# Kernel optimization log

Measured on AMD Instinct MI355X. Metric: run time of the kernel, lower is better.

Reference implementation:

```python
import jax, jax.numpy as jnp
import numpy as np

N = 50000      # nodes
E = 800000     # edges (avg degree 16)
D = 128        # d_model
C = 2          # num_classes
F_IN = 8       # GCNConv(8, d_model)


def setup_inputs() -> dict:
    key = jax.random.key(0)
    ks = jax.random.split(key, 12)
    s = 0.05  # weight init scale
    return {
        "feature_vec": jax.random.normal(ks[0], (N, F_IN), dtype=jnp.float32),
        "bboxes": jax.random.uniform(ks[1], (N, 4), dtype=jnp.float32),
        "bbox_indices": jnp.arange(N, dtype=jnp.int64) if jax.config.jax_enable_x64 else jnp.arange(N, dtype=jnp.int32),
        "edge_index": jax.random.randint(ks[2], (2, E), 0, N, dtype=jnp.int32),
        "W1": jax.random.normal(ks[3], (F_IN, D), dtype=jnp.float32) * s,
        "b1": jnp.zeros((D,), dtype=jnp.float32),
        "W2": jax.random.normal(ks[4], (D, D), dtype=jnp.float32) * s,
        "b2": jnp.zeros((D,), dtype=jnp.float32),
        "lin1_W": jax.random.normal(ks[5], (2 * D, D), dtype=jnp.float32) * s,
        "lin1_b": jnp.zeros((D,), dtype=jnp.float32),
        "linf_W": jax.random.normal(ks[6], (D, C), dtype=jnp.float32) * s,
        "linf_b": jnp.zeros((C,), dtype=jnp.float32),
    }


def gcn_conv(x, W, b, edge_index, n):
    """PyG GCNConv: add self-loops, symmetric D^-1/2 A D^-1/2 normalization."""
    x = x @ W                                   # [n, out]
    sl = jnp.arange(n, dtype=edge_index.dtype)
    row = jnp.concatenate([edge_index[0], sl])  # source
    col = jnp.concatenate([edge_index[1], sl])  # target
    ones = jnp.ones(row.shape[0], dtype=x.dtype)
    deg = jax.ops.segment_sum(ones, col, num_segments=n)  # >= 1 due to self-loops
    dinv = jax.lax.rsqrt(deg)
    norm = dinv[row] * dinv[col]                # [E + n]
    msg = x[row] * norm[:, None]                # gather + scale
    out = jax.ops.segment_sum(msg, col, num_segments=n)   # scatter-aggregate
    return out + b


def reference(feature_vec, bboxes, bbox_indices, edge_index,
              W1, b1, W2, b2, lin1_W, lin1_b, linf_W, linf_b):
    n = feature_vec.shape[0]
    x = jax.nn.relu(gcn_conv(feature_vec, W1, b1, edge_index, n))
    x = jax.nn.relu(gcn_conv(x, W2, b2, edge_index, n))
    x1 = x[edge_index[0]]                        # [E, D]
    x2 = x[edge_index[1]]                        # [E, D]
    xpair = jnp.concatenate([x1, x2], axis=-1)   # [E, 2D]
    xpair = jax.nn.relu(xpair @ lin1_W + lin1_b)
    xfin = xpair @ linf_W + linf_b               # [E, C]
    probs = jax.nn.log_softmax(xfin, axis=-1)
    bbox_pairs = jnp.concatenate([bboxes[edge_index[0]], bboxes[edge_index[1]]], axis=-1)  # [E, 8]
    bbox_index_pairs = jnp.stack([bbox_indices[edge_index[0]], bbox_indices[edge_index[1]]], axis=1)  # [E, 2]
    return (probs, bbox_pairs, bbox_index_pairs)
```

## Files before the change

### kernel.cpp

```cpp
#include <hip/hip_runtime.h>
#include <hip/hip_bf16.h>
#include <math.h>


typedef __attribute__((ext_vector_type(8))) short short8;
typedef __attribute__((ext_vector_type(4))) float f32x4;
typedef __attribute__((ext_vector_type(2))) float fv2;

__device__ inline ushort f2bf(float f) {
    union { __hip_bfloat16 h; ushort u; } cv;
    cv.h = __float2bfloat16(f);
    return cv.u;
}
__device__ inline float bf2f(ushort u) {
    union { float f; uint u; } c;
    c.u = ((uint)u) << 16;
    return c.f;
}
__device__ inline uchar f2fp8(float f) {
    uint p = __builtin_amdgcn_cvt_pk_fp8_f32(f, f, 0u, false);
    return (uchar)(p & 0xffu);
}

__global__ void k_hist(const int* __restrict__ col, int* __restrict__ cnt, int E) {
    int e = blockIdx.x * blockDim.x + threadIdx.x;
    if (e < E) atomicAdd(&cnt[col[e]], 1);
}

__global__ __launch_bounds__(1024) void k_bsum(const int* __restrict__ cnt,
                                               int* __restrict__ bsum, int N) {
    __shared__ int ts[1024];
    const int b = blockIdx.x, t = threadIdx.x;
    const int i0 = b * 2048 + 2 * t;
    int a0 = (i0 < N) ? cnt[i0] : 0;
    int a1 = (i0 + 1 < N) ? cnt[i0 + 1] : 0;
    ts[t] = a0 + a1;
    __syncthreads();
#pragma unroll
    for (int off = 512; off > 0; off >>= 1) {
        if (t < off) ts[t] += ts[t + off];
        __syncthreads();
    }
    if (t == 0) bsum[b] = ts[0];
}

__global__ __launch_bounds__(1024) void k_scanw(const int* __restrict__ cnt,
                                                const int* __restrict__ bsum,
                                                int* __restrict__ ptr, int N, int E) {
    __shared__ int ts[1024];
    const int b = blockIdx.x, t = threadIdx.x;
    int boff = 0;
    for (int i = 0; i < b; ++i) boff += bsum[i];
    const int i0 = b * 2048 + 2 * t;
    const int a0 = (i0 < N) ? cnt[i0] : 0;
    const int a1 = (i0 + 1 < N) ? cnt[i0 + 1] : 0;
    const int s = a0 + a1;
    ts[t] = s;
    __syncthreads();
    for (int off = 1; off < 1024; off <<= 1) {
        int v = (t >= off) ? ts[t - off] : 0;
        __syncthreads();
        ts[t] += v;
        __syncthreads();
    }
    const int excl = boff + ts[t] - s;
    if (i0 < N) ptr[i0] = excl;
    if (i0 + 1 < N) ptr[i0 + 1] = excl + a0;
    if (b == 0 && t == 0) ptr[N] = E;
}

__global__ void k_fill(const int* __restrict__ row, const int* __restrict__ col,
                       const int* __restrict__ cnt, const int* __restrict__ ptr,
                       int* __restrict__ cursor, int2* __restrict__ eadj, int E) {
    int e = blockIdx.x * blockDim.x + threadIdx.x;
    if (e >= E) return;
    int r = row[e], c = col[e];
    float dr = rsqrtf(1.0f + (float)cnt[r]);
    float dc = rsqrtf(1.0f + (float)cnt[c]);
    int p = ptr[c] + atomicAdd(&cursor[c], 1);
    eadj[p] = make_int2(r, __float_as_int(dr * dc));
}

__global__ void k_prepWuv(const float* __restrict__ W, ushort* __restrict__ Wuv) {
    int tid = blockIdx.x * blockDim.x + threadIdx.x;
    if (tid >= 256 * 128) return;
    int c = tid >> 7, k = tid & 127;
    int krow = k + ((c >> 7) << 7);
    Wuv[tid] = f2bf(W[krow * 128 + (c & 127)]);
}
__global__ void k_prepW2(const float* __restrict__ W, ushort* __restrict__ Wt) {
    int tid = blockIdx.x * blockDim.x + threadIdx.x;
    if (tid >= 128 * 128) return;
    int n = tid >> 7, k = tid & 127;
    Wt[tid] = f2bf(W[k * 128 + n]);
}

__global__ __launch_bounds__(256) void k_agg8(const float* __restrict__ feat,
                                              const int* __restrict__ cnt,
                                              const int* __restrict__ ptr,
                                              const int2* __restrict__ eadj,
                                              float* __restrict__ aggF, int N) {
    int lane8 = threadIdx.x & 7;
    int node = blockIdx.x * 32 + (threadIdx.x >> 3);
    if (node >= N) return;
    float dd = 1.0f / (1.0f + (float)cnt[node]);
    float acc = feat[(size_t)node * 8 + lane8] * dd;
    int i = ptr[node], end = ptr[node + 1];
    for (; i < end; ++i) {
        const int2 a = eadj[i];
        acc += feat[(size_t)a.x * 8 + lane8] * __int_as_float(a.y);
    }
    aggF[(size_t)node * 8 + lane8] = acc;
}

__global__ __launch_bounds__(256) void k_gemm1(const float* __restrict__ aggF,
                                               const float* __restrict__ W1,
                                               const float* __restrict__ b1,
                                               ushort* __restrict__ x1, int total) {
    int tid = blockIdx.x * blockDim.x + threadIdx.x;
    if (tid >= total) return;
    int n = tid >> 7, j = tid & 127;
    float acc = b1[j];
#pragma unroll
    for (int k = 0; k < 8; ++k) acc += aggF[(size_t)n * 8 + k] * W1[k * 128 + j];
    x1[tid] = f2bf(fmaxf(acc, 0.f));
}

__global__ __launch_bounds__(256) void k_gemm2(const ushort* __restrict__ x1,
                                               const ushort* __restrict__ W2t,
                                               ushort* __restrict__ h2, int N) {
    __shared__ ushort ldsW[128 * 128];
    const int tid = threadIdx.x;
    const int wave = tid >> 6, lane = tid & 63;
    const int m = lane & 15, kb = lane >> 4;
    const int n0 = blockIdx.x * 64;

    const int node_a = min(n0 + wave * 16 + m, N - 1);
    short8 a[4];
#pragma unroll
    for (int kk = 0; kk < 4; ++kk) {
        a[kk] = *reinterpret_cast<const short8*>(&x1[(size_t)node_a * 128 + kk * 32 + kb * 8]);
    }

    {
        char* lb = reinterpret_cast<char*>(ldsW);
        const short8* wg = reinterpret_cast<const short8*>(W2t);
#pragma unroll
        for (int i = 0; i < 8; ++i) {
            const int g = i * 256 + tid;
            const int bo = g * 16;
            const int swz = bo ^ (((bo >> 8) & 7) << 4);
            *reinterpret_cast<short8*>(lb + swz) = wg[g];
        }
    }
    __syncthreads();

    f32x4 acc[8];
#pragma unroll
    for (int t = 0; t < 8; ++t) acc[t] = (f32x4){0.f, 0.f, 0.f, 0.f};

    const char* lbr = reinterpret_cast<const char*>(ldsW);
    const int mswz = (m & 7) << 4;
#pragma unroll
    for (int kk = 0; kk < 4; ++kk) {
#pragma unroll
        for (int t = 0; t < 8; ++t) {
            const int bo = (t * 16 + m) * 256 + kk * 64 + kb * 16;
            const short8 b = *reinterpret_cast<const short8*>(lbr + (bo ^ mswz));
            acc[t] = __builtin_amdgcn_mfma_f32_16x16x32_bf16(a[kk], b, acc[t], 0, 0, 0);
        }
    }

#pragma unroll
    for (int r = 0; r < 4; ++r) {
        const int node = n0 + wave * 16 + kb * 4 + r;
        if (node < N) {
#pragma unroll
            for (int t = 0; t < 8; ++t) {
                h2[(size_t)node * 128 + t * 16 + m] = f2bf(acc[t][r]);
            }
        }
    }
}

__global__ __launch_bounds__(256) void k_gather2(const ushort* __restrict__ h2,
                                                 const int* __restrict__ cnt,
                                                 const int* __restrict__ ptr,
                                                 const int2* __restrict__ eadj,
                                                 const float* __restrict__ b2,
                                                 ushort* __restrict__ xbf, int N) {
    int lane16 = threadIdx.x & 15;
    int node = blockIdx.x * 16 + (threadIdx.x >> 4);
    if (node >= N) return;
    float dd = 1.0f / (1.0f + (float)cnt[node]);
    float acc[8];
    {
        const short8 v = *reinterpret_cast<const short8*>(&h2[(size_t)node * 128 + lane16 * 8]);
#pragma unroll
        for (int i = 0; i < 8; ++i) acc[i] = bf2f((ushort)v[i]) * dd;
    }
    int i = ptr[node], end = ptr[node + 1];
    for (; i < end; ++i) {
        const int2 aa = eadj[i];
        const int s = aa.x;
        const float nm = __int_as_float(aa.y);
        const short8 v = *reinterpret_cast<const short8*>(&h2[(size_t)s * 128 + lane16 * 8]);
#pragma unroll
        for (int q = 0; q < 8; ++q) acc[q] += bf2f((ushort)v[q]) * nm;
    }
    short8 r;
#pragma unroll
    for (int q = 0; q < 8; ++q) {
        r[q] = (short)f2bf(fmaxf(acc[q] + b2[lane16 * 8 + q], 0.f));
    }
    *reinterpret_cast<short8*>(&xbf[(size_t)node * 128 + lane16 * 8]) = r;
}

__global__ __launch_bounds__(512) void k_gemm_uv(const ushort* __restrict__ xbf,
                                                 const ushort* __restrict__ Wuv,
                                                 const float* __restrict__ lin1b,
                                                 uchar* __restrict__ uv, int N) {
    __shared__ ushort ldsW[256 * 128];
    const int tid = threadIdx.x;
    const int wave = tid >> 6, lane = tid & 63;
    const int m = lane & 15, kb = lane >> 4;
    const int ng = wave >> 1;
    const int ch = wave & 1;
    const int n0 = blockIdx.x * 64 + ng * 16;

    const int node_a = min(n0 + m, N - 1);
    short8 a[4];
#pragma unroll
    for (int kk = 0; kk < 4; ++kk) {
        a[kk] = *reinterpret_cast<const short8*>(&xbf[(size_t)node_a * 128 + kk * 32 + kb * 8]);
    }

    {
        char* lb = reinterpret_cast<char*>(ldsW);
        const short8* wg = reinterpret_cast<const short8*>(Wuv);
#pragma unroll
        for (int i = 0; i < 8; ++i) {
            const int g = i * 512 + tid;
            const int bo = g * 16;
            const int swz = bo ^ (((bo >> 8) & 7) << 4);
            *reinterpret_cast<short8*>(lb + swz) = wg[g];
        }
    }
    __syncthreads();

    f32x4 acc[8];
#pragma unroll
    for (int t = 0; t < 8; ++t) acc[t] = (f32x4){0.f, 0.f, 0.f, 0.f};

    const char* lbr = reinterpret_cast<const char*>(ldsW);
    const int mswz = (m & 7) << 4;
#pragma unroll
    for (int kk = 0; kk < 4; ++kk) {
#pragma unroll
        for (int t = 0; t < 8; ++t) {
            const int bo = (ch * 128 + t * 16 + m) * 256 + kk * 64 + kb * 16;
            const short8 b = *reinterpret_cast<const short8*>(lbr + (bo ^ mswz));
            acc[t] = __builtin_amdgcn_mfma_f32_16x16x32_bf16(a[kk], b, acc[t], 0, 0, 0);
        }
    }

#pragma unroll
    for (int r = 0; r < 4; ++r) {
        const int node = n0 + kb * 4 + r;
        if (node < N) {
#pragma unroll
            for (int t = 0; t < 8; ++t) {
                const int c = t * 16 + m;
                float av = acc[t][r];
                if (ch == 0) av += lin1b[c];
                uv[(size_t)node * 256 + ch * 128 + c] = f2fp8(av);
            }
        }
    }
}

__global__ __launch_bounds__(256) void k_edge_lite(const uchar* __restrict__ uv,
                                                   const float* __restrict__ linfW,
                                                   const float* __restrict__ linfb,
                                                   const float* __restrict__ bboxes,
                                                   const int* __restrict__ bidx,
                                                   const int* __restrict__ row,
                                                   const int* __restrict__ col,
                                                   float* __restrict__ out_probs,
                                                   float* __restrict__ out_bbox,
                                                   float* __restrict__ out_bidx,
                                                   int E) {
    const int lane8 = threadIdx.x & 7;
    const int slot = threadIdx.x >> 3;
    int e = blockIdx.x * 32 + slot;
    if (e >= E) return;

    float wd[16];
#pragma unroll
    for (int j = 0; j < 16; ++j) {
        const int c = lane8 * 16 + j;
        wd[j] = linfW[c * 2] - linfW[c * 2 + 1];
    }
    const float bias_d = linfb[0] - linfb[1];
    const int step = gridDim.x * 32;

    int s = row[e], d = col[e];
    uint4 ua = *reinterpret_cast<const uint4*>(&uv[(size_t)s * 256 + lane8 * 16]);
    uint4 va = *reinterpret_cast<const uint4*>(&uv[(size_t)d * 256 + 128 + lane8 * 16]);

    while (true) {
        const int e2 = e + step;
        const bool more = (e2 < E);
        int s2 = 0, d2 = 0;
        uint4 ua2 = ua, va2 = va;
        if (more) {
            s2 = row[e2];
            d2 = col[e2];
            ua2 = *reinterpret_cast<const uint4*>(&uv[(size_t)s2 * 256 + lane8 * 16]);
            va2 = *reinterpret_cast<const uint4*>(&uv[(size_t)d2 * 256 + 128 + lane8 * 16]);
        }

        float p = 0.f;
        {
            const uint uw[4] = {ua.x, ua.y, ua.z, ua.w};
            const uint vw[4] = {va.x, va.y, va.z, va.w};
#pragma unroll
            for (int w = 0; w < 4; ++w) {
                const fv2 ul = __builtin_amdgcn_cvt_pk_f32_fp8(uw[w], false);
                const fv2 uh = __builtin_amdgcn_cvt_pk_f32_fp8(uw[w], true);
                const fv2 vl = __builtin_amdgcn_cvt_pk_f32_fp8(vw[w], false);
                const fv2 vh = __builtin_amdgcn_cvt_pk_f32_fp8(vw[w], true);
                p = fmaf(fmaxf(ul[0] + vl[0], 0.f), wd[4 * w + 0], p);
                p = fmaf(fmaxf(ul[1] + vl[1], 0.f), wd[4 * w + 1], p);
                p = fmaf(fmaxf(uh[0] + vh[0], 0.f), wd[4 * w + 2], p);
                p = fmaf(fmaxf(uh[1] + vh[1], 0.f), wd[4 * w + 3], p);
            }
        }
        p += __shfl_xor(p, 1);
        p += __shfl_xor(p, 2);
        p += __shfl_xor(p, 4);

        out_bbox[(size_t)e * 8 + lane8] = bboxes[(size_t)((lane8 < 4) ? s : d) * 4 + (lane8 & 3)];
        if (lane8 == 0) {
            *reinterpret_cast<float2*>(&out_bidx[(size_t)e * 2]) =
                make_float2((float)bidx[s], (float)bidx[d]);
        } else if (lane8 == 1) {
            const float dd = p + bias_d;
            const float ad = fabsf(dd);
            const float t = -log1pf(expf(-ad));
            const float2 pr = (dd >= 0.f) ? make_float2(t, t - ad) : make_float2(t - ad, t);
            *reinterpret_cast<float2*>(&out_probs[(size_t)e * 2]) = pr;
        }

        if (!more) break;
        e = e2; s = s2; d = d2; ua = ua2; va = va2;
    }
}

extern "C" void kernel_launch(void* const* d_in, const int* in_sizes, int n_in,
                              void* d_out, int out_size, void* d_ws, size_t ws_size,
                              hipStream_t stream) {
    const float* feat   = (const float*)d_in[0];
    const float* bboxes = (const float*)d_in[1];
    const int*   bidx   = (const int*)d_in[2];
    const int*   eidx   = (const int*)d_in[3];
    const float* W1     = (const float*)d_in[4];
    const float* b1     = (const float*)d_in[5];
    const float* W2     = (const float*)d_in[6];
    const float* b2     = (const float*)d_in[7];
    const float* lin1W  = (const float*)d_in[8];
    const float* lin1b  = (const float*)d_in[9];
    const float* linfW  = (const float*)d_in[10];
    const float* linfb  = (const float*)d_in[11];

    const int N = in_sizes[0] / 8;
    const int E = in_sizes[3] / 2;
    const int* row = eidx;
    const int* col = eidx + E;

    size_t Np = ((size_t)N + 255) & ~255ull;
    size_t Ep = ((size_t)E + 255) & ~255ull;
    size_t A8 = (((size_t)N * 8) + 255) & ~255ull;
    int*    cnt    = (int*)d_ws;
    int*    cursor = cnt + Np;
    int*    ptr    = cursor + Np;
    int*    bsum   = ptr + Np + 256;
    int2*   eadj   = (int2*)(bsum + 256);
    float*  aggF   = (float*)(eadj + Ep);
    ushort* x1     = (ushort*)(aggF + A8);
    ushort* h2     = x1 + (size_t)N * 128;
    uchar*  uvbuf  = (uchar*)(h2 + (size_t)N * 128);
    ushort* Wuv    = (ushort*)(uvbuf + (size_t)N * 256);
    ushort* W2t    = Wuv + 256 * 128;
    ushort* xbf    = x1;

    float* out       = (float*)d_out;
    float* out_probs = out;
    float* out_bbox  = out + (size_t)E * 2;
    float* out_bidx  = out + (size_t)E * 10;

    const int total = N * 128;
    const int B = 256;
    const int nchunk = (N + 2047) / 2048;

    hipMemsetAsync(cnt, 0, 2 * Np * sizeof(int), stream);
    k_hist<<<(E + B - 1) / B, B, 0, stream>>>(col, cnt, E);
    k_bsum<<<nchunk, 1024, 0, stream>>>(cnt, bsum, N);
    k_scanw<<<nchunk, 1024, 0, stream>>>(cnt, bsum, ptr, N, E);
    k_fill<<<(E + B - 1) / B, B, 0, stream>>>(row, col, cnt, ptr, cursor, eadj, E);
    k_prepWuv<<<(256 * 128 + B - 1) / B, B, 0, stream>>>(lin1W, Wuv);
    k_prepW2<<<(128 * 128 + B - 1) / B, B, 0, stream>>>(W2, W2t);

    k_agg8<<<(N + 31) / 32, B, 0, stream>>>(feat, cnt, ptr, eadj, aggF, N);
    k_gemm1<<<(total + B - 1) / B, B, 0, stream>>>(aggF, W1, b1, x1, total);

    k_gemm2<<<(N + 63) / 64, B, 0, stream>>>(x1, W2t, h2, N);
    k_gather2<<<(N + 15) / 16, B, 0, stream>>>(h2, cnt, ptr, eadj, b2, xbf, N);

    k_gemm_uv<<<(N + 63) / 64, 512, 0, stream>>>(xbf, Wuv, lin1b, uvbuf, N);

    k_edge_lite<<<2048, B, 0, stream>>>(uvbuf, linfW, linfb,
                                        bboxes, bidx, row, col,
                                        out_probs, out_bbox, out_bidx, E);
}
```

Baseline: 248.1 us.

## Store layer-2 pre-aggregation features as fp8 and fuse layer-1 aggregation with GEMM

The intermediate h2 (x@W2) is now stored as fp8 instead of bf16, which halves the bytes read by the neighbor-gather in k_gather2. That kernel is remapped so 8 lanes per node each handle 16 channels, with packed fp8-to-f32 conversion. The layer-1 aggregation and its 8x128 matmul are fused into one kernel that keeps W1 in LDS, dropping the aggF round trip. The two weight-prep kernels are merged into one launch. The fp8 storage lowers precision of the layer-2 messages and could hurt accuracy tolerance.

Measured after the change: 219.1 us. 1.13x faster.

```diff
diff --git a/kernel.cpp b/kernel.cpp
--- a/kernel.cpp
+++ b/kernel.cpp
@@ -81,54 +81,70 @@
     eadj[p] = make_int2(r, __float_as_int(dr * dc));
 }
 
-__global__ void k_prepWuv(const float* __restrict__ W, ushort* __restrict__ Wuv) {
+__global__ void k_prepW(const float* __restrict__ lin1W, const float* __restrict__ W2,
+                        ushort* __restrict__ Wuv, ushort* __restrict__ W2t) {
     int tid = blockIdx.x * blockDim.x + threadIdx.x;
-    if (tid >= 256 * 128) return;
-    int c = tid >> 7, k = tid & 127;
-    int krow = k + ((c >> 7) << 7);
-    Wuv[tid] = f2bf(W[krow * 128 + (c & 127)]);
-}
-__global__ void k_prepW2(const float* __restrict__ W, ushort* __restrict__ Wt) {
-    int tid = blockIdx.x * blockDim.x + threadIdx.x;
-    if (tid >= 128 * 128) return;
-    int n = tid >> 7, k = tid & 127;
-    Wt[tid] = f2bf(W[k * 128 + n]);
-}
-
-__global__ __launch_bounds__(256) void k_agg8(const float* __restrict__ feat,
-                                              const int* __restrict__ cnt,
-                                              const int* __restrict__ ptr,
-                                              const int2* __restrict__ eadj,
-                                              float* __restrict__ aggF, int N) {
-    int lane8 = threadIdx.x & 7;
-    int node = blockIdx.x * 32 + (threadIdx.x >> 3);
-    if (node >= N) return;
-    float dd = 1.0f / (1.0f + (float)cnt[node]);
-    float acc = feat[(size_t)node * 8 + lane8] * dd;
-    int i = ptr[node], end = ptr[node + 1];
-    for (; i < end; ++i) {
-        const int2 a = eadj[i];
-        acc += feat[(size_t)a.x * 8 + lane8] * __int_as_float(a.y);
-    }
-    aggF[(size_t)node * 8 + lane8] = acc;
-}
-
-__global__ __launch_bounds__(256) void k_gemm1(const float* __restrict__ aggF,
-                                               const float* __restrict__ W1,
-                                               const float* __restrict__ b1,
-                                               ushort* __restrict__ x1, int total) {
-    int tid = blockIdx.x * blockDim.x + threadIdx.x;
-    if (tid >= total) return;
-    int n = tid >> 7, j = tid & 127;
-    float acc = b1[j];
-#pragma unroll
-    for (int k = 0; k < 8; ++k) acc += aggF[(size_t)n * 8 + k] * W1[k * 128 + j];
-    x1[tid] = f2bf(fmaxf(acc, 0.f));
+    if (tid < 256 * 128) {
+        int c = tid >> 7, k = tid & 127;
+        int krow = k + ((c >> 7) << 7);
+        Wuv[tid] = f2bf(lin1W[krow * 128 + (c & 127)]);
+    } else if (tid < 256 * 128 + 128 * 128) {
+        int u = tid - 256 * 128;
+        int n = u >> 7, k = u & 127;
+        W2t[u] = f2bf(W2[k * 128 + n]);
+    }
+}
+
+__global__ __launch_bounds__(256) void k_l1(const float* __restrict__ feat,
+                                            const int* __restrict__ cnt,
+                                            const int* __restrict__ ptr,
+                                            const int2* __restrict__ eadj,
+                                            const float* __restrict__ W1,
+                                            const float* __restrict__ b1,
+                                            ushort* __restrict__ x1, int N) {
+    __shared__ float sagg[32][8];
+    __shared__ float sW1[8 * 128];
+    const int tid = threadIdx.x;
+    for (int i = tid; i < 1024; i += 256) sW1[i] = W1[i];
+
+    const int lane8 = tid & 7;
+    const int nloc = tid >> 3;
+    const int node = blockIdx.x * 32 + nloc;
+    float acc = 0.f;
+    if (node < N) {
+        float dd = 1.0f / (1.0f + (float)cnt[node]);
+        acc = feat[(size_t)node * 8 + lane8] * dd;
+        int i = ptr[node], end = ptr[node + 1];
+        for (; i < end; ++i) {
+            const int2 a = eadj[i];
+            acc += feat[(size_t)a.x * 8 + lane8] * __int_as_float(a.y);
+        }
+    }
+    sagg[nloc][lane8] = acc;
+    __syncthreads();
+
+    if (node < N) {
+        const int jb = lane8 * 16;
+        float av[8];
+#pragma unroll
+        for (int k = 0; k < 8; ++k) av[k] = sagg[nloc][k];
+        short8 r0, r1;
+#pragma unroll
+        for (int j = 0; j < 16; ++j) {
+            float s = b1[jb + j];
+#pragma unroll
+            for (int k = 0; k < 8; ++k) s = fmaf(av[k], sW1[k * 128 + jb + j], s);
+            const ushort bv = f2bf(fmaxf(s, 0.f));
+            if (j < 8) r0[j] = (short)bv; else r1[j - 8] = (short)bv;
+        }
+        *reinterpret_cast<short8*>(&x1[(size_t)node * 128 + jb]) = r0;
+        *reinterpret_cast<short8*>(&x1[(size_t)node * 128 + jb + 8]) = r1;
+    }
 }
 
 __global__ __launch_bounds__(256) void k_gemm2(const ushort* __restrict__ x1,
                                                const ushort* __restrict__ W2t,
-                                               ushort* __restrict__ h2, int N) {
+                                               uchar* __restrict__ h2, int N) {
     __shared__ ushort ldsW[128 * 128];
     const int tid = threadIdx.x;
     const int wave = tid >> 6, lane = tid & 63;
@@ -177,43 +193,61 @@
         if (node < N) {
 #pragma unroll
             for (int t = 0; t < 8; ++t) {
-                h2[(size_t)node * 128 + t * 16 + m] = f2bf(acc[t][r]);
+                h2[(size_t)node * 128 + t * 16 + m] = f2fp8(acc[t][r]);
             }
         }
     }
 }
 
-__global__ __launch_bounds__(256) void k_gather2(const ushort* __restrict__ h2,
+__global__ __launch_bounds__(256) void k_gather2(const uchar* __restrict__ h2,
                                                  const int* __restrict__ cnt,
                                                  const int* __restrict__ ptr,
                                                  const int2* __restrict__ eadj,
                                                  const float* __restrict__ b2,
                                                  ushort* __restrict__ xbf, int N) {
-    int lane16 = threadIdx.x & 15;
-    int node = blockIdx.x * 16 + (threadIdx.x >> 4);
+    const int lane8 = threadIdx.x & 7;
+    const int node = blockIdx.x * 32 + (threadIdx.x >> 3);
     if (node >= N) return;
-    float dd = 1.0f / (1.0f + (float)cnt[node]);
-    float acc[8];
+    const float dd = 1.0f / (1.0f + (float)cnt[node]);
+    float acc[16];
     {
-        const short8 v = *reinterpret_cast<const short8*>(&h2[(size_t)node * 128 + lane16 * 8]);
-#pragma unroll
-        for (int i = 0; i < 8; ++i) acc[i] = bf2f((ushort)v[i]) * dd;
-    }
-    int i = ptr[node], end = ptr[node + 1];
+        const uint4 w = *reinterpret_cast<const uint4*>(&h2[(size_t)node * 128 + lane8 * 16]);
+        const uint ws[4] = {w.x, w.y, w.z, w.w};
+#pragma unroll
+        for (int q = 0; q < 4; ++q) {
+            const fv2 lo = __builtin_amdgcn_cvt_pk_f32_fp8(ws[q], false);
+            const fv2 hi = __builtin_amdgcn_cvt_pk_f32_fp8(ws[q], true);
+            acc[4 * q + 0] = lo[0] * dd;
+            acc[4 * q + 1] = lo[1] * dd;
+            acc[4 * q + 2] = hi[0] * dd;
+            acc[4 * q + 3] = hi[1] * dd;
+        }
+    }
+    int i = ptr[node];
+    const int end = ptr[node + 1];
     for (; i < end; ++i) {
         const int2 aa = eadj[i];
-        const int s = aa.x;
         const float nm = __int_as_float(aa.y);
-        const short8 v = *reinterpret_cast<const short8*>(&h2[(size_t)s * 128 + lane16 * 8]);
-#pragma unroll
-        for (int q = 0; q < 8; ++q) acc[q] += bf2f((ushort)v[q]) * nm;
-    }
-    short8 r;
+        const uint4 w = *reinterpret_cast<const uint4*>(&h2[(size_t)aa.x * 128 + lane8 * 16]);
+        const uint ws[4] = {w.x, w.y, w.z, w.w};
+#pragma unroll
+        for (int q = 0; q < 4; ++q) {
+            const fv2 lo = __builtin_amdgcn_cvt_pk_f32_fp8(ws[q], false);
+            const fv2 hi = __builtin_amdgcn_cvt_pk_f32_fp8(ws[q], true);
+            acc[4 * q + 0] = fmaf(lo[0], nm, acc[4 * q + 0]);
+            acc[4 * q + 1] = fmaf(lo[1], nm, acc[4 * q + 1]);
+            acc[4 * q + 2] = fmaf(hi[0], nm, acc[4 * q + 2]);
+            acc[4 * q + 3] = fmaf(hi[1], nm, acc[4 * q + 3]);
+        }
+    }
+    short8 r0, r1;
 #pragma unroll
     for (int q = 0; q < 8; ++q) {
-        r[q] = (short)f2bf(fmaxf(acc[q] + b2[lane16 * 8 + q], 0.f));
-    }
-    *reinterpret_cast<short8*>(&xbf[(size_t)node * 128 + lane16 * 8]) = r;
+        r0[q] = (short)f2bf(fmaxf(acc[q] + b2[lane8 * 16 + q], 0.f));
+        r1[q] = (short)f2bf(fmaxf(acc[8 + q] + b2[lane8 * 16 + 8 + q], 0.f));
+    }
+    *reinterpret_cast<short8*>(&xbf[(size_t)node * 128 + lane8 * 16]) = r0;
+    *reinterpret_cast<short8*>(&xbf[(size_t)node * 128 + lane8 * 16 + 8]) = r1;
 }
 
 __global__ __launch_bounds__(512) void k_gemm_uv(const ushort* __restrict__ xbf,
@@ -380,16 +414,14 @@
 
     size_t Np = ((size_t)N + 255) & ~255ull;
     size_t Ep = ((size_t)E + 255) & ~255ull;
-    size_t A8 = (((size_t)N * 8) + 255) & ~255ull;
     int*    cnt    = (int*)d_ws;
     int*    cursor = cnt + Np;
     int*    ptr    = cursor + Np;
     int*    bsum   = ptr + Np + 256;
     int2*   eadj   = (int2*)(bsum + 256);
-    float*  aggF   = (float*)(eadj + Ep);
-    ushort* x1     = (ushort*)(aggF + A8);
-    ushort* h2     = x1 + (size_t)N * 128;
-    uchar*  uvbuf  = (uchar*)(h2 + (size_t)N * 128);
+    ushort* x1     = (ushort*)(eadj + Ep);
+    uchar*  h2     = (uchar*)(x1 + (size_t)N * 128);
+    uchar*  uvbuf  = h2 + (size_t)N * 128;
     ushort* Wuv    = (ushort*)(uvbuf + (size_t)N * 256);
     ushort* W2t    = Wuv + 256 * 128;
     ushort* xbf    = x1;
@@ -399,7 +431,6 @@
     float* out_bbox  = out + (size_t)E * 2;
     float* out_bidx  = out + (size_t)E * 10;
 
-    const int total = N * 128;
     const int B = 256;
     const int nchunk = (N + 2047) / 2048;
 
@@ -408,14 +439,12 @@
     k_bsum<<<nchunk, 1024, 0, stream>>>(cnt, bsum, N);
     k_scanw<<<nchunk, 1024, 0, stream>>>(cnt, bsum, ptr, N, E);
     k_fill<<<(E + B - 1) / B, B, 0, stream>>>(row, col, cnt, ptr, cursor, eadj, E);
-    k_prepWuv<<<(256 * 128 + B - 1) / B, B, 0, stream>>>(lin1W, Wuv);
-    k_prepW2<<<(128 * 128 + B - 1) / B, B, 0, stream>>>(W2, W2t);
-
-    k_agg8<<<(N + 31) / 32, B, 0, stream>>>(feat, cnt, ptr, eadj, aggF, N);
-    k_gemm1<<<(total + B - 1) / B, B, 0, stream>>>(aggF, W1, b1, x1, total);
+    k_prepW<<<(256 * 128 + 128 * 128 + B - 1) / B, B, 0, stream>>>(lin1W, W2, Wuv, W2t);
+
+    k_l1<<<(N + 31) / 32, B, 0, stream>>>(feat, cnt, ptr, eadj, W1, b1, x1, N);
 
     k_gemm2<<<(N + 63) / 64, B, 0, stream>>>(x1, W2t, h2, N);
-    k_gather2<<<(N + 15) / 16, B, 0, stream>>>(h2, cnt, ptr, eadj, b2, xbf, N);
+    k_gather2<<<(N + 31) / 32, B, 0, stream>>>(h2, cnt, ptr, eadj, b2, xbf, N);
 
     k_gemm_uv<<<(N + 63) / 64, 512, 0, stream>>>(xbf, Wuv, lin1b, uvbuf, N);
 
```
